# Optimization experiments

Measured on AMD Instinct MI355X. Metric: run time of the kernel, lower is better.

Reference implementation:

```python
import jax, jax.numpy as jnp
import numpy as np

N = 100_000   # nodes
E = 1_600_000 # edges (avg degree 16)
B = 512       # graphs in batch
F_IN = 64; H = 4; D = 64; HD = H * D; EXTRA = 16
NEG_SLOPE = 0.2  # DGL GATConv default


def _gat_conv(x, src, dst, W, al, ar, bias):
    """DGL GATConv: fc -> per-head attn logits -> edge leaky_relu -> segment softmax over dst -> scatter-sum."""
    h = (x @ W).reshape(N, H, D)                       # [N,H,D]
    el = jnp.sum(h * al, axis=-1)                      # [N,H]
    er = jnp.sum(h * ar, axis=-1)                      # [N,H]
    e = jax.nn.leaky_relu(el[src] + er[dst], NEG_SLOPE)  # [E,H]
    m = jax.ops.segment_max(e, dst, num_segments=N)    # [N,H]
    m = jnp.where(jnp.isfinite(m), m, 0.0)             # guard empty segments
    ex = jnp.exp(e - m[dst])                           # [E,H]
    den = jax.ops.segment_sum(ex, dst, num_segments=N) # [N,H]
    alpha = ex / jnp.maximum(den[dst], 1e-9)           # [E,H]
    msg = h[src] * alpha[:, :, None]                   # [E,H,D]
    out = jax.ops.segment_sum(msg, dst, num_segments=N) + bias.reshape(1, H, D)
    return out  # [N,H,D]


def setup_inputs() -> dict:
    key = jax.random.key(0)
    ks = jax.random.split(key, 26)
    nrm = lambda k, shape: jax.random.normal(k, shape, dtype=jnp.float32) * 0.5
    src = jax.random.randint(ks[0], (E,), 0, N)
    # ensure every node has >=1 incoming edge (DGL disallows zero in-degree by default)
    dst = jnp.concatenate([jnp.arange(N), jax.random.randint(ks[1], (E - N,), 0, N)])
    node_graph = jnp.sort(jax.random.randint(ks[2], (N,), 0, B))
    inp = dict(
        src=src, dst=dst, node_graph=node_graph,
        feats_node=jax.random.normal(ks[3], (N, F_IN), dtype=jnp.float32),
        feats_graph=jax.random.normal(ks[4], (B, EXTRA), dtype=jnp.float32),
        W1=nrm(ks[5], (F_IN, HD)), al1=nrm(ks[6], (H, D)), ar1=nrm(ks[7], (H, D)), bg1=jnp.zeros(HD),
        W2=nrm(ks[8], (HD, HD)),  al2=nrm(ks[9], (H, D)), ar2=nrm(ks[10], (H, D)), bg2=jnp.zeros(HD),
        W3=nrm(ks[11], (HD, HD)), al3=nrm(ks[12], (H, D)), ar3=nrm(ks[13], (H, D)), bg3=jnp.zeros(HD),
        sw=nrm(ks[14], (HD, 1)), sb=jnp.zeros(1),
        lw1=nrm(ks[15], (HD + EXTRA, 2 * D)), lb1=jnp.zeros(2 * D),
        lw2=nrm(ks[16], (2 * D, D)), lb2=jnp.zeros(D),
        lw3=nrm(ks[17], (D, 1)), lb3=jnp.zeros(1),
    )
    return inp


def reference(src, dst, node_graph, feats_node, feats_graph,
              W1, al1, ar1, bg1, W2, al2, ar2, bg2, W3, al3, ar3, bg3,
              sw, sb, lw1, lb1, lw2, lb2, lw3, lb3):
    selu = jax.nn.selu
    x = selu(_gat_conv(feats_node, src, dst, W1, al1, ar1, bg1)).reshape(N, HD)
    x = selu(_gat_conv(x, src, dst, W2, al2, ar2, bg2)).reshape(N, HD)
    x = selu(_gat_conv(x, src, dst, W3, al3, ar3, bg3)).reshape(N, HD)
    # WeightedAverage readout: sigmoid-scored weighted mean per graph
    w = jax.nn.sigmoid(x @ sw + sb)                               # [N,1]
    num = jax.ops.segment_sum(w * x, node_graph, num_segments=B)  # [B,HD]
    den = jax.ops.segment_sum(w, node_graph, num_segments=B)      # [B,1]
    emb = num / jnp.maximum(den, 1e-9)
    y = jnp.concatenate([emb, feats_graph], axis=1)
    y = selu(y @ lw1 + lb1)
    y = selu(y @ lw2 + lb2)
    return y @ lw3 + lb3  # [B,1]
```

## Files before the change

### kernel.cpp

```cpp
#include <hip/hip_runtime.h>

#define N_NODES 100000
#define N_EDGES 1600000
#define N_GRAPHS 512
#define F_IN 64
#define HD 256
#define EXTRA 16
#define SCAN_BLOCK 512

typedef float f32x4 __attribute__((ext_vector_type(4)));
typedef _Float16 f16x4 __attribute__((ext_vector_type(4)));
typedef _Float16 f16x8 __attribute__((ext_vector_type(8)));

__device__ __forceinline__ float selu_f(float x) {
    const float a = 1.6732632423543772f, sc = 1.0507009873554805f;
    return x > 0.f ? sc * x : sc * a * (__expf(x) - 1.f);
}

__global__ __launch_bounds__(256) void hist_k(const int* __restrict__ dst, int* __restrict__ hist) {
    int j = blockIdx.x * 256 + threadIdx.x;
    if (j < N_EDGES) atomicAdd(&hist[dst[j]], 1);
}

__global__ __launch_bounds__(SCAN_BLOCK) void scan1_k(const int* __restrict__ hist,
                                                      int* __restrict__ row_ptr,
                                                      int* __restrict__ bsums) {
    __shared__ int sm[SCAN_BLOCK];
    int t = threadIdx.x;
    int i = blockIdx.x * SCAN_BLOCK + t;
    int v = (i < N_NODES) ? hist[i] : 0;
    sm[t] = v;
    __syncthreads();
    for (int off = 1; off < SCAN_BLOCK; off <<= 1) {
        int add = (t >= off) ? sm[t - off] : 0;
        __syncthreads();
        sm[t] += add;
        __syncthreads();
    }
    if (i < N_NODES) row_ptr[i] = sm[t] - v;
    if (t == SCAN_BLOCK - 1) bsums[blockIdx.x] = sm[t];
}

__global__ __launch_bounds__(256) void scan2_k(int* __restrict__ bsums, int nb) {
    __shared__ int sm[256];
    int t = threadIdx.x;
    int v = (t < nb) ? bsums[t] : 0;
    sm[t] = v;
    __syncthreads();
    for (int off = 1; off < 256; off <<= 1) {
        int add = (t >= off) ? sm[t - off] : 0;
        __syncthreads();
        sm[t] += add;
        __syncthreads();
    }
    if (t < nb) bsums[t] = sm[t] - v;
}

__global__ __launch_bounds__(256) void scan3_k(int* __restrict__ row_ptr, const int* __restrict__ bsums,
                                               int* __restrict__ cursor) {
    int i = blockIdx.x * 256 + threadIdx.x;
    if (i < N_NODES) {
        int r = row_ptr[i] + bsums[i / SCAN_BLOCK];
        row_ptr[i] = r;
        cursor[i] = r;
    }
    if (i == 0) row_ptr[N_NODES] = N_EDGES;
}

__global__ __launch_bounds__(256) void scatter_k(const int* __restrict__ src,
                                                 const int* __restrict__ dst,
                                                 int* __restrict__ cursor,
                                                 int* __restrict__ csr_src) {
    int j = blockIdx.x * 256 + threadIdx.x;
    if (j < N_EDGES) {
        int r = atomicAdd(&cursor[dst[j]], 1);
        csr_src[r] = src[j];
    }
}

__global__ __launch_bounds__(256) void gbound_k(const int* __restrict__ node_graph, int* __restrict__ gstart) {
    int g = blockIdx.x * 256 + threadIdx.x;
    if (g > N_GRAPHS) return;
    int lo = 0, hi = N_NODES;
    while (lo < hi) {
        int mid = (lo + hi) >> 1;
        if (node_graph[mid] < g) lo = mid + 1; else hi = mid;
    }
    gstart[g] = lo;
}

__global__ __launch_bounds__(256) void tcast_split_k(const float* __restrict__ W,
                                                     _Float16* __restrict__ Wt_hi,
                                                     _Float16* __restrict__ Wt_lo, int K) {
    int idx = blockIdx.x * 256 + threadIdx.x;
    if (idx >= K * HD) return;
    int n = idx / K, k = idx - n * K;
    float w = W[(size_t)k * HD + n];
    _Float16 hi = (_Float16)w;
    _Float16 lo = (_Float16)(w - (float)hi);
    Wt_hi[idx] = hi;
    Wt_lo[idx] = lo;
}

__global__ __launch_bounds__(256) void split_cast_k(const float* __restrict__ in,
                                                    _Float16* __restrict__ hi,
                                                    _Float16* __restrict__ lo, int n4) {
    int i = blockIdx.x * 256 + threadIdx.x;
    if (i >= n4) return;
    float4 v = *(const float4*)(in + (size_t)i * 4);
    f16x4 h, l;
    h.x = (_Float16)v.x; l.x = (_Float16)(v.x - (float)h.x);
    h.y = (_Float16)v.y; l.y = (_Float16)(v.y - (float)h.y);
    h.z = (_Float16)v.z; l.z = (_Float16)(v.z - (float)h.z);
    h.w = (_Float16)v.w; l.w = (_Float16)(v.w - (float)h.w);
    *(f16x4*)(hi + (size_t)i * 4) = h;
    *(f16x4*)(lo + (size_t)i * 4) = l;
}

template <int K>
__global__ __launch_bounds__(256) void gemm_split_k(const _Float16* __restrict__ Ahi,
                                                    const _Float16* __restrict__ Alo,
                                                    const _Float16* __restrict__ Bt_hi,
                                                    const _Float16* __restrict__ Bt_lo,
                                                    const float* __restrict__ al,
                                                    const float* __restrict__ ar,
                                                    _Float16* __restrict__ Chi,
                                                    float* __restrict__ el,
                                                    float* __restrict__ er, int M) {
    const int BM = 128, BN = 128, LDP = 40;
    __shared__ _Float16 As_hi[BM][LDP];
    __shared__ _Float16 As_lo[BM][LDP];
    __shared__ _Float16 Bs_hi[BN][LDP];
    __shared__ _Float16 Bs_lo[BN][LDP];
    int tid = threadIdx.x;
    int wave = tid >> 6, lane = tid & 63;
    int q = lane >> 4, l16 = lane & 15;
    int row0 = blockIdx.y * BM, col0 = blockIdx.x * BN;
    f32x4 acc[2][8] = {};

    for (int k0 = 0; k0 < K; k0 += 32) {
#pragma unroll
        for (int c = 0; c < 2; c++) {
            int cc = tid + c * 256;
            int r = cc >> 2, o = (cc & 3) * 8;
            int gr = row0 + r;
            f16x8 vh = {}, vl = {};
            if (gr < M) {
                vh = *(const f16x8*)(Ahi + (size_t)gr * K + k0 + o);
                vl = *(const f16x8*)(Alo + (size_t)gr * K + k0 + o);
            }
            *(f16x8*)&As_hi[r][o] = vh;
            *(f16x8*)&As_lo[r][o] = vl;
        }
#pragma unroll
        for (int c = 0; c < 2; c++) {
            int cc = tid + c * 256;
            int n = cc >> 2, o = (cc & 3) * 8;
            *(f16x8*)&Bs_hi[n][o] = *(const f16x8*)(Bt_hi + (size_t)(col0 + n) * K + k0 + o);
            *(f16x8*)&Bs_lo[n][o] = *(const f16x8*)(Bt_lo + (size_t)(col0 + n) * K + k0 + o);
        }
        __syncthreads();

        f16x8 ah[2], alo2[2];
#pragma unroll
        for (int ms = 0; ms < 2; ms++) {
            int m = wave * 32 + ms * 16 + l16;
            ah[ms] = *(const f16x8*)&As_hi[m][q * 8];
            alo2[ms] = *(const f16x8*)&As_lo[m][q * 8];
        }
#pragma unroll
        for (int ns = 0; ns < 8; ns++) {
            int n = ns * 16 + l16;
            f16x8 bh = *(const f16x8*)&Bs_hi[n][q * 8];
            f16x8 bl = *(const f16x8*)&Bs_lo[n][q * 8];
#pragma unroll
            for (int ms = 0; ms < 2; ms++) {
                acc[ms][ns] = __builtin_amdgcn_mfma_f32_16x16x32_f16(ah[ms], bh, acc[ms][ns], 0, 0, 0);
                acc[ms][ns] = __builtin_amdgcn_mfma_f32_16x16x32_f16(ah[ms], bl, acc[ms][ns], 0, 0, 0);
                acc[ms][ns] = __builtin_amdgcn_mfma_f32_16x16x32_f16(alo2[ms], bh, acc[ms][ns], 0, 0, 0);
            }
        }
        __syncthreads();
    }

    const int h0 = col0 >> 6;
    float alv[8], arv[8];
#pragma unroll
    for (int ns = 0; ns < 8; ns++) {
        int hh = h0 + (ns >> 2);
        int d = (ns & 3) * 16 + l16;
        alv[ns] = al[hh * 64 + d];
        arv[ns] = ar[hh * 64 + d];
    }
#pragma unroll
    for (int ms = 0; ms < 2; ms++) {
#pragma unroll
        for (int i = 0; i < 4; i++) {
            int r = row0 + wave * 32 + ms * 16 + q * 4 + i;
            bool ok = r < M;
            float el0 = 0.f, er0 = 0.f, el1 = 0.f, er1 = 0.f;
#pragma unroll
            for (int ns = 0; ns < 8; ns++) {
                float v = acc[ms][ns][i];
                if (ok) Chi[(size_t)r * HD + col0 + ns * 16 + l16] = (_Float16)v;
                if (ns < 4) { el0 = fmaf(v, alv[ns], el0); er0 = fmaf(v, arv[ns], er0); }
                else        { el1 = fmaf(v, alv[ns], el1); er1 = fmaf(v, arv[ns], er1); }
            }
#pragma unroll
            for (int off = 1; off < 16; off <<= 1) {
                el0 += __shfl_xor(el0, off, 64);
                er0 += __shfl_xor(er0, off, 64);
                el1 += __shfl_xor(el1, off, 64);
                er1 += __shfl_xor(er1, off, 64);
            }
            if (l16 == 0 && ok) {
                el[(size_t)r * 4 + h0] = el0;
                el[(size_t)r * 4 + h0 + 1] = el1;
                er[(size_t)r * 4 + h0] = er0;
                er[(size_t)r * 4 + h0 + 1] = er1;
            }
        }
    }
}

template <int OUT>
__global__ __launch_bounds__(256) void gat_aggregate_k(const _Float16* __restrict__ hb,
                                                       const float* __restrict__ el,
                                                       const float* __restrict__ er,
                                                       const int* __restrict__ csr_src,
                                                       const int* __restrict__ row_ptr,
                                                       const float* __restrict__ bias,
                                                       _Float16* __restrict__ xhi,
                                                       _Float16* __restrict__ xlo,
                                                       float* __restrict__ xf32,
                                                       const float* __restrict__ sw,
                                                       const float* __restrict__ sb,
                                                       float* __restrict__ wsc) {
    __shared__ float wlds[4][64][4];
    __shared__ int snlds[4][64];
    int wv = threadIdx.x >> 6;
    int lane = threadIdx.x & 63;
    int v = blockIdx.x * 4 + wv;
    bool valid = v < N_NODES;
    int vc = valid ? v : 0;
    int rs = row_ptr[vc];
    int deg = valid ? row_ptr[vc + 1] - rs : 0;
    float4 erv = make_float4(0.f, 0.f, 0.f, 0.f);
    if (valid) erv = *(const float4*)(er + (size_t)vc * 4);

    int head = lane >> 4;
    float inv_den = 1.f;
    float m_h = 0.f, er_h = 0.f;
    f16x4 hv_pre[8];
    int nb0 = 0;

    if (deg <= 64) {
        float e0 = -1e30f, e1 = -1e30f, e2 = -1e30f, e3 = -1e30f;
        int my_sn = 0;
        if (lane < deg) {
            my_sn = csr_src[rs + lane];
            float4 elv = *(const float4*)(el + (size_t)my_sn * 4);
            float t0 = elv.x + erv.x, t1 = elv.y + erv.y, t2 = elv.z + erv.z, t3 = elv.w + erv.w;
            e0 = t0 > 0.f ? t0 : 0.2f * t0;
            e1 = t1 > 0.f ? t1 : 0.2f * t1;
            e2 = t2 > 0.f ? t2 : 0.2f * t2;
            e3 = t3 > 0.f ? t3 : 0.2f * t3;
        }
        nb0 = deg < 8 ? deg : 8;
#pragma unroll
        for (int u = 0; u < 8; u++) {
            int snb = __shfl(my_sn, u, 64);
            if (u < nb0) hv_pre[u] = *(const f16x4*)(hb + (size_t)snb * HD + lane * 4);
        }
        float m0 = e0, m1 = e1, m2 = e2, m3 = e3;
        for (int off = 1; off < deg; off <<= 1) {
            m0 = fmaxf(m0, __shfl_xor(m0, off, 64));
            m1 = fmaxf(m1, __shfl_xor(m1, off, 64));
            m2 = fmaxf(m2, __shfl_xor(m2, off, 64));
            m3 = fmaxf(m3, __shfl_xor(m3, off, 64));
        }
        float p0 = 0.f, p1 = 0.f, p2 = 0.f, p3 = 0.f;
        if (lane < deg) {
            p0 = __expf(e0 - m0); p1 = __expf(e1 - m1);
            p2 = __expf(e2 - m2); p3 = __expf(e3 - m3);
        }
        float s0 = p0, s1 = p1, s2 = p2, s3 = p3;
        for (int off = 1; off < deg; off <<= 1) {
            s0 += __shfl_xor(s0, off, 64);
            s1 += __shfl_xor(s1, off, 64);
            s2 += __shfl_xor(s2, off, 64);
            s3 += __shfl_xor(s3, off, 64);
        }
        float d0 = __shfl(s0, 0, 64), d1 = __shfl(s1, 0, 64);
        float d2 = __shfl(s2, 0, 64), d3 = __shfl(s3, 0, 64);
        float den = head == 0 ? d0 : head == 1 ? d1 : head == 2 ? d2 : d3;
        inv_den = 1.f / fmaxf(den, 1e-9f);
        if (lane < deg) {
            wlds[wv][lane][0] = p0;
            wlds[wv][lane][1] = p1;
            wlds[wv][lane][2] = p2;
            wlds[wv][lane][3] = p3;
            snlds[wv][lane] = my_sn;
        }
    } else {
        float m[4] = {-1e30f, -1e30f, -1e30f, -1e30f};
        float s[4] = {0.f, 0.f, 0.f, 0.f};
        for (int t = lane; t < deg; t += 64) {
            int sn = csr_src[rs + t];
            float4 elv = *(const float4*)(el + (size_t)sn * 4);
            float e[4];
            e[0] = elv.x + erv.x; e[1] = elv.y + erv.y; e[2] = elv.z + erv.z; e[3] = elv.w + erv.w;
#pragma unroll
            for (int hh = 0; hh < 4; hh++) {
                float ev = e[hh] > 0.f ? e[hh] : 0.2f * e[hh];
                float mn = fmaxf(m[hh], ev);
                s[hh] = s[hh] * __expf(m[hh] - mn) + __expf(ev - mn);
                m[hh] = mn;
            }
        }
#pragma unroll
        for (int off = 32; off >= 1; off >>= 1) {
#pragma unroll
            for (int hh = 0; hh < 4; hh++) {
                float mo = __shfl_xor(m[hh], off, 64);
                float so = __shfl_xor(s[hh], off, 64);
                float mn = fmaxf(m[hh], mo);
                s[hh] = s[hh] * __expf(m[hh] - mn) + so * __expf(mo - mn);
                m[hh] = mn;
            }
        }
        m_h = head == 0 ? m[0] : head == 1 ? m[1] : head == 2 ? m[2] : m[3];
        float den = head == 0 ? s[0] : head == 1 ? s[1] : head == 2 ? s[2] : s[3];
        er_h = head == 0 ? erv.x : head == 1 ? erv.y : head == 2 ? erv.z : erv.w;
        inv_den = 1.f / fmaxf(den, 1e-9f);
    }

    float a0 = 0.f, a1 = 0.f, a2 = 0.f, a3 = 0.f;
    if (deg <= 64) {
#pragma unroll
        for (int u = 0; u < 8; u++) {
            if (u < nb0) {
                float w = wlds[wv][u][head];
                a0 = fmaf(w, (float)hv_pre[u].x, a0);
                a1 = fmaf(w, (float)hv_pre[u].y, a1);
                a2 = fmaf(w, (float)hv_pre[u].z, a2);
                a3 = fmaf(w, (float)hv_pre[u].w, a3);
            }
        }
        int t = 8;
        for (; t + 8 <= deg; t += 8) {
            int sn[8];
            float w[8];
#pragma unroll
            for (int u = 0; u < 8; u++) {
                sn[u] = snlds[wv][t + u];
                w[u] = wlds[wv][t + u][head];
            }
            f16x4 hv[8];
#pragma unroll
            for (int u = 0; u < 8; u++)
                hv[u] = *(const f16x4*)(hb + (size_t)sn[u] * HD + lane * 4);
#pragma unroll
            for (int u = 0; u < 8; u++) {
                a0 = fmaf(w[u], (float)hv[u].x, a0);
                a1 = fmaf(w[u], (float)hv[u].y, a1);
                a2 = fmaf(w[u], (float)hv[u].z, a2);
                a3 = fmaf(w[u], (float)hv[u].w, a3);
            }
        }
        for (; t < deg; t++) {
            int sn = snlds[wv][t];
            float w = wlds[wv][t][head];
            f16x4 hv = *(const f16x4*)(hb + (size_t)sn * HD + lane * 4);
            a0 = fmaf(w, (float)hv.x, a0);
            a1 = fmaf(w, (float)hv.y, a1);
            a2 = fmaf(w, (float)hv.z, a2);
            a3 = fmaf(w, (float)hv.w, a3);
        }
    } else {
        for (int t = 0; t < deg; t++) {
            int sn = csr_src[rs + t];
            float e = el[(size_t)sn * 4 + head] + er_h;
            e = e > 0.f ? e : 0.2f * e;
            float w = __expf(e - m_h);
            f16x4 hv = *(const f16x4*)(hb + (size_t)sn * HD + lane * 4);
            a0 = fmaf(w, (float)hv.x, a0);
            a1 = fmaf(w, (float)hv.y, a1);
            a2 = fmaf(w, (float)hv.z, a2);
            a3 = fmaf(w, (float)hv.w, a3);
        }
    }
    float4 bv = *(const float4*)(bias + lane * 4);
    float4 o;
    o.x = selu_f(fmaf(a0, inv_den, bv.x));
    o.y = selu_f(fmaf(a1, inv_den, bv.y));
    o.z = selu_f(fmaf(a2, inv_den, bv.z));
    o.w = selu_f(fmaf(a3, inv_den, bv.w));

    if constexpr (OUT == 0) {
        f16x4 oh, ol;
        oh.x = (_Float16)o.x; ol.x = (_Float16)(o.x - (float)oh.x);
        oh.y = (_Float16)o.y; ol.y = (_Float16)(o.y - (float)oh.y);
        oh.z = (_Float16)o.z; ol.z = (_Float16)(o.z - (float)oh.z);
        oh.w = (_Float16)o.w; ol.w = (_Float16)(o.w - (float)oh.w);
        if (valid) {
            *(f16x4*)(xhi + (size_t)v * HD + lane * 4) = oh;
            *(f16x4*)(xlo + (size_t)v * HD + lane * 4) = ol;
        }
    } else {
        if (valid) *(float4*)(xf32 + (size_t)v * HD + lane * 4) = o;
        float4 sv = *(const float4*)(sw + lane * 4);
        float p = o.x * sv.x + o.y * sv.y + o.z * sv.z + o.w * sv.w;
#pragma unroll
        for (int off = 1; off < 64; off <<= 1) p += __shfl_xor(p, off, 64);
        if (lane == 0 && valid) wsc[v] = 1.f / (1.f + __expf(-(p + sb[0])));
    }
}

__global__ __launch_bounds__(256) void readout_k(const float* __restrict__ x,
                                                 const float* __restrict__ wsc,
                                                 const int* __restrict__ gstart,
                                                 const float* __restrict__ fg,
                                                 float* __restrict__ y0) {
    int g = blockIdx.x;
    int f = threadIdx.x;
    int s = gstart[g], e = gstart[g + 1];
    float num = 0.f, den = 0.f;
#pragma unroll 4
    for (int n = s; n < e; n++) {
        float wn = wsc[n];
        num = fmaf(wn, x[(size_t)n * HD + f], num);
        den += wn;
    }
    float emb = num / fmaxf(den, 1e-9f);
    y0[(size_t)g * 272 + f] = emb;
    if (f < EXTRA) y0[(size_t)g * 272 + 256 + f] = fg[g * EXTRA + f];
}

__global__ __launch_bounds__(128) void mlp_k(const float* __restrict__ y0g,
                                             const float* __restrict__ lw1, const float* __restrict__ lb1,
                                             const float* __restrict__ lw2, const float* __restrict__ lb2,
                                             const float* __restrict__ lw3, const float* __restrict__ lb3,
                                             float* __restrict__ out) {
    __shared__ float y0s[272];
    __shared__ float y1s[128];
    int g = blockIdx.x, t = threadIdx.x;
    for (int i = t; i < 272; i += 128) y0s[i] = y0g[(size_t)g * 272 + i];
    __syncthreads();
    float acc = lb1[t];
    for (int k = 0; k < 272; k++) acc = fmaf(y0s[k], lw1[k * 128 + t], acc);
    y1s[t] = selu_f(acc);
    __syncthreads();
    if (t < 64) {
        float a2 = lb2[t];
        for (int k = 0; k < 128; k++) a2 = fmaf(y1s[k], lw2[k * 64 + t], a2);
        float v2 = selu_f(a2);
        float p = v2 * lw3[t];
#pragma unroll
        for (int off = 1; off < 64; off <<= 1) p += __shfl_xor(p, off, 64);
        if (t == 0) out[g] = p + lb3[0];
    }
}

extern "C" void kernel_launch(void* const* d_in, const int* in_sizes, int n_in,
                              void* d_out, int out_size, void* d_ws, size_t ws_size,
                              hipStream_t stream) {
    const int* src = (const int*)d_in[0];
    const int* dst = (const int*)d_in[1];
    const int* node_graph = (const int*)d_in[2];
    const float* feats_node = (const float*)d_in[3];
    const float* feats_graph = (const float*)d_in[4];
    const float* W1 = (const float*)d_in[5];
    const float* al1 = (const float*)d_in[6];
    const float* ar1 = (const float*)d_in[7];
    const float* bg1 = (const float*)d_in[8];
    const float* W2 = (const float*)d_in[9];
    const float* al2 = (const float*)d_in[10];
    const float* ar2 = (const float*)d_in[11];
    const float* bg2 = (const float*)d_in[12];
    const float* W3 = (const float*)d_in[13];
    const float* al3 = (const float*)d_in[14];
    const float* ar3 = (const float*)d_in[15];
    const float* bg3 = (const float*)d_in[16];
    const float* sw = (const float*)d_in[17];
    const float* sb = (const float*)d_in[18];
    const float* lw1 = (const float*)d_in[19];
    const float* lb1 = (const float*)d_in[20];
    const float* lw2 = (const float*)d_in[21];
    const float* lb2 = (const float*)d_in[22];
    const float* lw3 = (const float*)d_in[23];
    const float* lb3 = (const float*)d_in[24];
    float* out = (float*)d_out;

    char* ws = (char*)d_ws;
    size_t off = 0;
    auto alloc = [&](size_t bytes) -> char* {
        char* p = ws + off;
        off += (bytes + 255) & ~(size_t)255;
        return p;
    };
    _Float16* xhi = (_Float16*)alloc((size_t)N_NODES * HD * 2);
    _Float16* xlo = (_Float16*)alloc((size_t)N_NODES * HD * 2);
    float* xf32 = (float*)xhi;
    _Float16* hhi = (_Float16*)alloc((size_t)N_NODES * HD * 2);
    _Float16* fhi = (_Float16*)alloc((size_t)N_NODES * F_IN * 2);
    _Float16* flo = (_Float16*)alloc((size_t)N_NODES * F_IN * 2);
    _Float16* W1hi = (_Float16*)alloc((size_t)F_IN * HD * 2);
    _Float16* W1lo = (_Float16*)alloc((size_t)F_IN * HD * 2);
    _Float16* W2hi = (_Float16*)alloc((size_t)HD * HD * 2);
    _Float16* W2lo = (_Float16*)alloc((size_t)HD * HD * 2);
    _Float16* W3hi = (_Float16*)alloc((size_t)HD * HD * 2);
    _Float16* W3lo = (_Float16*)alloc((size_t)HD * HD * 2);
    float* el = (float*)alloc((size_t)N_NODES * 4 * 4);
    float* er = (float*)alloc((size_t)N_NODES * 4 * 4);
    float* wsc = (float*)alloc((size_t)N_NODES * 4);
    float* y0 = (float*)alloc((size_t)N_GRAPHS * 272 * 4);
    int* hist = (int*)alloc((size_t)N_NODES * 4);
    int* row_ptr = (int*)alloc((size_t)(N_NODES + 1) * 4);
    int* cursor = (int*)alloc((size_t)N_NODES * 4);
    int* csr_src = (int*)alloc((size_t)N_EDGES * 4);
    int* gstart = (int*)alloc((size_t)(N_GRAPHS + 1) * 4);
    int* bsums = (int*)alloc(256 * 4);
    (void)ws_size; (void)in_sizes; (void)n_in; (void)out_size;

    hipMemsetAsync(hist, 0, (size_t)N_NODES * 4, stream);

    hist_k<<<(N_EDGES + 255) / 256, 256, 0, stream>>>(dst, hist);
    int nb = (N_NODES + SCAN_BLOCK - 1) / SCAN_BLOCK;
    scan1_k<<<nb, SCAN_BLOCK, 0, stream>>>(hist, row_ptr, bsums);
    scan2_k<<<1, 256, 0, stream>>>(bsums, nb);
    scan3_k<<<(N_NODES + 255) / 256, 256, 0, stream>>>(row_ptr, bsums, cursor);
    scatter_k<<<(N_EDGES + 255) / 256, 256, 0, stream>>>(src, dst, cursor, csr_src);
    gbound_k<<<3, 256, 0, stream>>>(node_graph, gstart);

    split_cast_k<<<(N_NODES * F_IN / 4 + 255) / 256, 256, 0, stream>>>(feats_node, fhi, flo, N_NODES * F_IN / 4);
    tcast_split_k<<<(F_IN * HD + 255) / 256, 256, 0, stream>>>(W1, W1hi, W1lo, F_IN);
    tcast_split_k<<<(HD * HD + 255) / 256, 256, 0, stream>>>(W2, W2hi, W2lo, HD);
    tcast_split_k<<<(HD * HD + 255) / 256, 256, 0, stream>>>(W3, W3hi, W3lo, HD);

    dim3 ggrid(HD / 128, (N_NODES + 127) / 128);
    int nwb = (N_NODES + 3) / 4;

    gemm_split_k<F_IN><<<ggrid, 256, 0, stream>>>(fhi, flo, W1hi, W1lo, al1, ar1, hhi, el, er, N_NODES);
    gat_aggregate_k<0><<<nwb, 256, 0, stream>>>(hhi, el, er, csr_src, row_ptr, bg1, xhi, xlo, nullptr, nullptr, nullptr, nullptr);
    gemm_split_k<HD><<<ggrid, 256, 0, stream>>>(xhi, xlo, W2hi, W2lo, al2, ar2, hhi, el, er, N_NODES);
    gat_aggregate_k<0><<<nwb, 256, 0, stream>>>(hhi, el, er, csr_src, row_ptr, bg2, xhi, xlo, nullptr, nullptr, nullptr, nullptr);
    gemm_split_k<HD><<<ggrid, 256, 0, stream>>>(xhi, xlo, W3hi, W3lo, al3, ar3, hhi, el, er, N_NODES);
    gat_aggregate_k<1><<<nwb, 256, 0, stream>>>(hhi, el, er, csr_src, row_ptr, bg3, nullptr, nullptr, xf32, sw, sb, wsc);

    readout_k<<<N_GRAPHS, 256, 0, stream>>>(xf32, wsc, gstart, feats_graph, y0);
    mlp_k<<<N_GRAPHS, 128, 0, stream>>>(y0, lw1, lb1, lw2, lb2, lw3, lb3, out);
}
```

Baseline: 952.8 us.

## Split wavefront into two half-waves gathering 16-byte neighbor rows per edge

The aggregation kernel now has each half of the 64-lane wavefront handle alternate edges, with each lane loading 8 fp16 features (16 bytes) per neighbor instead of 4. The two half-wave partial sums are combined with a cross-half shuffle, and the output stores are split between the halves. This doubles the edges in flight per wavefront and widens the per-lane gather loads, aimed at the latency-bound neighbor gather. In exchange it drops the explicit 8-edge prefetch that overlapped with the softmax reductions, and it doubles the accumulator registers.

```diff
diff --git a/kernel.cpp b/kernel.cpp
--- a/kernel.cpp
+++ b/kernel.cpp
@@ -240,6 +240,9 @@
     __shared__ int snlds[4][64];
     int wv = threadIdx.x >> 6;
     int lane = threadIdx.x & 63;
+    int p = lane >> 5;
+    int l = lane & 31;
+    int head_l = l >> 3;
     int v = blockIdx.x * 4 + wv;
     bool valid = v < N_NODES;
     int vc = valid ? v : 0;
@@ -248,13 +251,11 @@
     float4 erv = make_float4(0.f, 0.f, 0.f, 0.f);
     if (valid) erv = *(const float4*)(er + (size_t)vc * 4);
 
-    int head = lane >> 4;
     float inv_den = 1.f;
-    float m_h = 0.f, er_h = 0.f;
-    f16x4 hv_pre[8];
-    int nb0 = 0;
-
-    if (deg <= 64) {
+    bool fast = deg <= 64;
+    float acc[8] = {};
+
+    if (fast) {
         float e0 = -1e30f, e1 = -1e30f, e2 = -1e30f, e3 = -1e30f;
         int my_sn = 0;
         if (lane < deg) {
@@ -266,12 +267,6 @@
             e2 = t2 > 0.f ? t2 : 0.2f * t2;
             e3 = t3 > 0.f ? t3 : 0.2f * t3;
         }
-        nb0 = deg < 8 ? deg : 8;
-#pragma unroll
-        for (int u = 0; u < 8; u++) {
-            int snb = __shfl(my_sn, u, 64);
-            if (u < nb0) hv_pre[u] = *(const f16x4*)(hb + (size_t)snb * HD + lane * 4);
-        }
         float m0 = e0, m1 = e1, m2 = e2, m3 = e3;
         for (int off = 1; off < deg; off <<= 1) {
             m0 = fmaxf(m0, __shfl_xor(m0, off, 64));
@@ -293,7 +288,7 @@
         }
         float d0 = __shfl(s0, 0, 64), d1 = __shfl(s1, 0, 64);
         float d2 = __shfl(s2, 0, 64), d3 = __shfl(s3, 0, 64);
-        float den = head == 0 ? d0 : head == 1 ? d1 : head == 2 ? d2 : d3;
+        float den = head_l == 0 ? d0 : head_l == 1 ? d1 : head_l == 2 ? d2 : d3;
         inv_den = 1.f / fmaxf(den, 1e-9f);
         if (lane < deg) {
             wlds[wv][lane][0] = p0;
@@ -301,6 +296,19 @@
             wlds[wv][lane][2] = p2;
             wlds[wv][lane][3] = p3;
             snlds[wv][lane] = my_sn;
+        }
+
+#pragma unroll 8
+        for (int t = 0; t < deg; t += 2) {
+            int e = t + p;
+            bool act = e < deg;
+            int ei = act ? e : 0;
+            int sn = snlds[wv][ei];
+            float w = act ? wlds[wv][ei][head_l] : 0.f;
+            f16x8 hv = *(const f16x8*)(hb + (size_t)sn * HD + l * 8);
+#pragma unroll
+            for (int i = 0; i < 8; i++)
+                acc[i] = fmaf(w, (float)hv[i], acc[i]);
         }
     } else {
         float m[4] = {-1e30f, -1e30f, -1e30f, -1e30f};
@@ -329,91 +337,71 @@
                 m[hh] = mn;
             }
         }
-        m_h = head == 0 ? m[0] : head == 1 ? m[1] : head == 2 ? m[2] : m[3];
-        float den = head == 0 ? s[0] : head == 1 ? s[1] : head == 2 ? s[2] : s[3];
-        er_h = head == 0 ? erv.x : head == 1 ? erv.y : head == 2 ? erv.z : erv.w;
+        float m_h = head_l == 0 ? m[0] : head_l == 1 ? m[1] : head_l == 2 ? m[2] : m[3];
+        float den = head_l == 0 ? s[0] : head_l == 1 ? s[1] : head_l == 2 ? s[2] : s[3];
+        float er_h = head_l == 0 ? erv.x : head_l == 1 ? erv.y : head_l == 2 ? erv.z : erv.w;
         inv_den = 1.f / fmaxf(den, 1e-9f);
-    }
-
-    float a0 = 0.f, a1 = 0.f, a2 = 0.f, a3 = 0.f;
-    if (deg <= 64) {
-#pragma unroll
-        for (int u = 0; u < 8; u++) {
-            if (u < nb0) {
-                float w = wlds[wv][u][head];
-                a0 = fmaf(w, (float)hv_pre[u].x, a0);
-                a1 = fmaf(w, (float)hv_pre[u].y, a1);
-                a2 = fmaf(w, (float)hv_pre[u].z, a2);
-                a3 = fmaf(w, (float)hv_pre[u].w, a3);
-            }
-        }
-        int t = 8;
-        for (; t + 8 <= deg; t += 8) {
-            int sn[8];
-            float w[8];
-#pragma unroll
-            for (int u = 0; u < 8; u++) {
-                sn[u] = snlds[wv][t + u];
-                w[u] = wlds[wv][t + u][head];
-            }
-            f16x4 hv[8];
-#pragma unroll
-            for (int u = 0; u < 8; u++)
-                hv[u] = *(const f16x4*)(hb + (size_t)sn[u] * HD + lane * 4);
-#pragma unroll
-            for (int u = 0; u < 8; u++) {
-                a0 = fmaf(w[u], (float)hv[u].x, a0);
-                a1 = fmaf(w[u], (float)hv[u].y, a1);
-                a2 = fmaf(w[u], (float)hv[u].z, a2);
-                a3 = fmaf(w[u], (float)hv[u].w, a3);
-            }
-        }
-        for (; t < deg; t++) {
-            int sn = snlds[wv][t];
-            float w = wlds[wv][t][head];
-            f16x4 hv = *(const f16x4*)(hb + (size_t)sn * HD + lane * 4);
-            a0 = fmaf(w, (float)hv.x, a0);
-            a1 = fmaf(w, (float)hv.y, a1);
-            a2 = fmaf(w, (float)hv.z, a2);
-            a3 = fmaf(w, (float)hv.w, a3);
+        for (int t = 0; t < deg; t += 2) {
+            int e = t + p;
+            bool act = e < deg;
+            int sn = csr_src[rs + (act ? e : 0)];
+            float4 elv = *(const float4*)(el + (size_t)sn * 4);
+            float eh = (head_l == 0 ? elv.x : head_l == 1 ? elv.y : head_l == 2 ? elv.z : elv.w) + er_h;
+            eh = eh > 0.f ? eh : 0.2f * eh;
+            float w = act ? __expf(eh - m_h) : 0.f;
+            f16x8 hv = *(const f16x8*)(hb + (size_t)sn * HD + l * 8);
+#pragma unroll
+            for (int i = 0; i < 8; i++)
+                acc[i] = fmaf(w, (float)hv[i], acc[i]);
+        }
+    }
+
+#pragma unroll
+    for (int i = 0; i < 8; i++)
+        acc[i] += __shfl_xor(acc[i], 32, 64);
+
+    float4 b0 = *(const float4*)(bias + l * 8);
+    float4 b1 = *(const float4*)(bias + l * 8 + 4);
+    float o[8];
+    o[0] = selu_f(fmaf(acc[0], inv_den, b0.x));
+    o[1] = selu_f(fmaf(acc[1], inv_den, b0.y));
+    o[2] = selu_f(fmaf(acc[2], inv_den, b0.z));
+    o[3] = selu_f(fmaf(acc[3], inv_den, b0.w));
+    o[4] = selu_f(fmaf(acc[4], inv_den, b1.x));
+    o[5] = selu_f(fmaf(acc[5], inv_den, b1.y));
+    o[6] = selu_f(fmaf(acc[6], inv_den, b1.z));
+    o[7] = selu_f(fmaf(acc[7], inv_den, b1.w));
+
+    if constexpr (OUT == 0) {
+        if (valid) {
+            if (p == 0) {
+                f16x8 oh;
+#pragma unroll
+                for (int i = 0; i < 8; i++) oh[i] = (_Float16)o[i];
+                *(f16x8*)(xhi + (size_t)v * HD + l * 8) = oh;
+            } else {
+                f16x8 ol;
+#pragma unroll
+                for (int i = 0; i < 8; i++) {
+                    _Float16 h = (_Float16)o[i];
+                    ol[i] = (_Float16)(o[i] - (float)h);
+                }
+                *(f16x8*)(xlo + (size_t)v * HD + l * 8) = ol;
+            }
         }
     } else {
-        for (int t = 0; t < deg; t++) {
-            int sn = csr_src[rs + t];
-            float e = el[(size_t)sn * 4 + head] + er_h;
-            e = e > 0.f ? e : 0.2f * e;
-            float w = __expf(e - m_h);
-            f16x4 hv = *(const f16x4*)(hb + (size_t)sn * HD + lane * 4);
-            a0 = fmaf(w, (float)hv.x, a0);
-            a1 = fmaf(w, (float)hv.y, a1);
-            a2 = fmaf(w, (float)hv.z, a2);
-            a3 = fmaf(w, (float)hv.w, a3);
-        }
-    }
-    float4 bv = *(const float4*)(bias + lane * 4);
-    float4 o;
-    o.x = selu_f(fmaf(a0, inv_den, bv.x));
-    o.y = selu_f(fmaf(a1, inv_den, bv.y));
-    o.z = selu_f(fmaf(a2, inv_den, bv.z));
-    o.w = selu_f(fmaf(a3, inv_den, bv.w));
-
-    if constexpr (OUT == 0) {
-        f16x4 oh, ol;
-        oh.x = (_Float16)o.x; ol.x = (_Float16)(o.x - (float)oh.x);
-        oh.y = (_Float16)o.y; ol.y = (_Float16)(o.y - (float)oh.y);
-        oh.z = (_Float16)o.z; ol.z = (_Float16)(o.z - (float)oh.z);
-        oh.w = (_Float16)o.w; ol.w = (_Float16)(o.w - (float)oh.w);
         if (valid) {
-            *(f16x4*)(xhi + (size_t)v * HD + lane * 4) = oh;
-            *(f16x4*)(xlo + (size_t)v * HD + lane * 4) = ol;
-        }
-    } else {
-        if (valid) *(float4*)(xf32 + (size_t)v * HD + lane * 4) = o;
-        float4 sv = *(const float4*)(sw + lane * 4);
-        float p = o.x * sv.x + o.y * sv.y + o.z * sv.z + o.w * sv.w;
-#pragma unroll
-        for (int off = 1; off < 64; off <<= 1) p += __shfl_xor(p, off, 64);
-        if (lane == 0 && valid) wsc[v] = 1.f / (1.f + __expf(-(p + sb[0])));
+            if (p == 0)
+                *(float4*)(xf32 + (size_t)v * HD + l * 8) = make_float4(o[0], o[1], o[2], o[3]);
+            else
+                *(float4*)(xf32 + (size_t)v * HD + l * 8 + 4) = make_float4(o[4], o[5], o[6], o[7]);
+        }
+        float4 sv = *(const float4*)(sw + l * 8 + 4 * p);
+        float ps = p == 0 ? (o[0] * sv.x + o[1] * sv.y + o[2] * sv.z + o[3] * sv.w)
+                          : (o[4] * sv.x + o[5] * sv.y + o[6] * sv.z + o[7] * sv.w);
+#pragma unroll
+        for (int off = 1; off < 64; off <<= 1) ps += __shfl_xor(ps, off, 64);
+        if (lane == 0 && valid) wsc[v] = 1.f / (1.f + __expf(-(ps + sb[0])));
     }
 }
 
```

Measured after the change: 966.3 us. No clear change (+1.4%).

## Fuse weighted readout into final aggregation and register-prefetch GEMM tiles

Applied to the files above, without the earlier changes.

The final GAT aggregation now computes the sigmoid score and accumulates weighted node features and weights per graph with atomics, reducing in shared memory when all four nodes in a block share a graph. This removes the fp32 node-feature write, the gstart binary search and the separate readout kernel. Separately, the split-fp16 GEMM prefetches the next K tile into registers while MFMAs run on the current tile. Atomics make the float sums order-nondeterministic and add memsets, and the prefetch adds an extra barrier per K step.

```diff
diff --git a/kernel.cpp b/kernel.cpp
--- a/kernel.cpp
+++ b/kernel.cpp
@@ -76,17 +76,6 @@
         int r = atomicAdd(&cursor[dst[j]], 1);
         csr_src[r] = src[j];
     }
-}
-
-__global__ __launch_bounds__(256) void gbound_k(const int* __restrict__ node_graph, int* __restrict__ gstart) {
-    int g = blockIdx.x * 256 + threadIdx.x;
-    if (g > N_GRAPHS) return;
-    int lo = 0, hi = N_NODES;
-    while (lo < hi) {
-        int mid = (lo + hi) >> 1;
-        if (node_graph[mid] < g) lo = mid + 1; else hi = mid;
-    }
-    gstart[g] = lo;
 }
 
 __global__ __launch_bounds__(256) void tcast_split_k(const float* __restrict__ W,
@@ -138,28 +127,43 @@
     int row0 = blockIdx.y * BM, col0 = blockIdx.x * BN;
     f32x4 acc[2][8] = {};
 
-    for (int k0 = 0; k0 < K; k0 += 32) {
+    int sr = tid >> 2, so = (tid & 3) * 8;
+    f16x8 rAh[2], rAl[2], rBh[2], rBl[2];
+
+    auto load_tile = [&](int k0) {
 #pragma unroll
         for (int c = 0; c < 2; c++) {
-            int cc = tid + c * 256;
-            int r = cc >> 2, o = (cc & 3) * 8;
+            int r = sr + 64 * c;
             int gr = row0 + r;
             f16x8 vh = {}, vl = {};
             if (gr < M) {
-                vh = *(const f16x8*)(Ahi + (size_t)gr * K + k0 + o);
-                vl = *(const f16x8*)(Alo + (size_t)gr * K + k0 + o);
-            }
-            *(f16x8*)&As_hi[r][o] = vh;
-            *(f16x8*)&As_lo[r][o] = vl;
-        }
+                vh = *(const f16x8*)(Ahi + (size_t)gr * K + k0 + so);
+                vl = *(const f16x8*)(Alo + (size_t)gr * K + k0 + so);
+            }
+            rAh[c] = vh; rAl[c] = vl;
+            int gb = col0 + r;
+            rBh[c] = *(const f16x8*)(Bt_hi + (size_t)gb * K + k0 + so);
+            rBl[c] = *(const f16x8*)(Bt_lo + (size_t)gb * K + k0 + so);
+        }
+    };
+    auto store_tile = [&]() {
 #pragma unroll
         for (int c = 0; c < 2; c++) {
-            int cc = tid + c * 256;
-            int n = cc >> 2, o = (cc & 3) * 8;
-            *(f16x8*)&Bs_hi[n][o] = *(const f16x8*)(Bt_hi + (size_t)(col0 + n) * K + k0 + o);
-            *(f16x8*)&Bs_lo[n][o] = *(const f16x8*)(Bt_lo + (size_t)(col0 + n) * K + k0 + o);
-        }
-        __syncthreads();
+            int r = sr + 64 * c;
+            *(f16x8*)&As_hi[r][so] = rAh[c];
+            *(f16x8*)&As_lo[r][so] = rAl[c];
+            *(f16x8*)&Bs_hi[r][so] = rBh[c];
+            *(f16x8*)&Bs_lo[r][so] = rBl[c];
+        }
+    };
+
+    load_tile(0);
+    store_tile();
+    __syncthreads();
+
+    for (int k0 = 0; k0 < K; k0 += 32) {
+        bool more = (k0 + 32) < K;
+        if (more) load_tile(k0 + 32);
 
         f16x8 ah[2], alo2[2];
 #pragma unroll
@@ -180,7 +184,11 @@
                 acc[ms][ns] = __builtin_amdgcn_mfma_f32_16x16x32_f16(alo2[ms], bh, acc[ms][ns], 0, 0, 0);
             }
         }
-        __syncthreads();
+        if (more) {
+            __syncthreads();
+            store_tile();
+            __syncthreads();
+        }
     }
 
     const int h0 = col0 >> 6;
@@ -232,10 +240,11 @@
                                                        const float* __restrict__ bias,
                                                        _Float16* __restrict__ xhi,
                                                        _Float16* __restrict__ xlo,
-                                                       float* __restrict__ xf32,
                                                        const float* __restrict__ sw,
                                                        const float* __restrict__ sb,
-                                                       float* __restrict__ wsc) {
+                                                       const int* __restrict__ node_graph,
+                                                       float* __restrict__ num,
+                                                       float* __restrict__ den) {
     __shared__ float wlds[4][64][4];
     __shared__ int snlds[4][64];
     int wv = threadIdx.x >> 6;
@@ -293,8 +302,8 @@
         }
         float d0 = __shfl(s0, 0, 64), d1 = __shfl(s1, 0, 64);
         float d2 = __shfl(s2, 0, 64), d3 = __shfl(s3, 0, 64);
-        float den = head == 0 ? d0 : head == 1 ? d1 : head == 2 ? d2 : d3;
-        inv_den = 1.f / fmaxf(den, 1e-9f);
+        float dh = head == 0 ? d0 : head == 1 ? d1 : head == 2 ? d2 : d3;
+        inv_den = 1.f / fmaxf(dh, 1e-9f);
         if (lane < deg) {
             wlds[wv][lane][0] = p0;
             wlds[wv][lane][1] = p1;
@@ -330,9 +339,9 @@
             }
         }
         m_h = head == 0 ? m[0] : head == 1 ? m[1] : head == 2 ? m[2] : m[3];
-        float den = head == 0 ? s[0] : head == 1 ? s[1] : head == 2 ? s[2] : s[3];
+        float dh = head == 0 ? s[0] : head == 1 ? s[1] : head == 2 ? s[2] : s[3];
         er_h = head == 0 ? erv.x : head == 1 ? erv.y : head == 2 ? erv.z : erv.w;
-        inv_den = 1.f / fmaxf(den, 1e-9f);
+        inv_den = 1.f / fmaxf(dh, 1e-9f);
     }
 
     float a0 = 0.f, a1 = 0.f, a2 = 0.f, a3 = 0.f;
@@ -408,36 +417,40 @@
             *(f16x4*)(xlo + (size_t)v * HD + lane * 4) = ol;
         }
     } else {
-        if (valid) *(float4*)(xf32 + (size_t)v * HD + lane * 4) = o;
+        __shared__ float bnum[4][256];
+        __shared__ float bden[4];
+        __shared__ int bg[4];
         float4 sv = *(const float4*)(sw + lane * 4);
-        float p = o.x * sv.x + o.y * sv.y + o.z * sv.z + o.w * sv.w;
-#pragma unroll
-        for (int off = 1; off < 64; off <<= 1) p += __shfl_xor(p, off, 64);
-        if (lane == 0 && valid) wsc[v] = 1.f / (1.f + __expf(-(p + sb[0])));
-    }
-}
-
-__global__ __launch_bounds__(256) void readout_k(const float* __restrict__ x,
-                                                 const float* __restrict__ wsc,
-                                                 const int* __restrict__ gstart,
-                                                 const float* __restrict__ fg,
-                                                 float* __restrict__ y0) {
-    int g = blockIdx.x;
-    int f = threadIdx.x;
-    int s = gstart[g], e = gstart[g + 1];
-    float num = 0.f, den = 0.f;
-#pragma unroll 4
-    for (int n = s; n < e; n++) {
-        float wn = wsc[n];
-        num = fmaf(wn, x[(size_t)n * HD + f], num);
-        den += wn;
-    }
-    float emb = num / fmaxf(den, 1e-9f);
-    y0[(size_t)g * 272 + f] = emb;
-    if (f < EXTRA) y0[(size_t)g * 272 + 256 + f] = fg[g * EXTRA + f];
-}
-
-__global__ __launch_bounds__(128) void mlp_k(const float* __restrict__ y0g,
+        float ps = o.x * sv.x + o.y * sv.y + o.z * sv.z + o.w * sv.w;
+#pragma unroll
+        for (int off = 1; off < 64; off <<= 1) ps += __shfl_xor(ps, off, 64);
+        float wn = valid ? 1.f / (1.f + __expf(-(ps + sb[0]))) : 0.f;
+        int g = valid ? node_graph[vc] : -1;
+        bnum[wv][lane * 4 + 0] = wn * o.x;
+        bnum[wv][lane * 4 + 1] = wn * o.y;
+        bnum[wv][lane * 4 + 2] = wn * o.z;
+        bnum[wv][lane * 4 + 3] = wn * o.w;
+        if (lane == 0) { bden[wv] = wn; bg[wv] = g; }
+        __syncthreads();
+        bool uni = (bg[0] == bg[1]) && (bg[1] == bg[2]) && (bg[2] == bg[3]) && (bg[0] >= 0);
+        if (uni) {
+            int t = threadIdx.x;
+            float s = bnum[0][t] + bnum[1][t] + bnum[2][t] + bnum[3][t];
+            atomicAdd(&num[(size_t)bg[0] * 256 + t], s);
+            if (t == 0) atomicAdd(&den[bg[0]], bden[0] + bden[1] + bden[2] + bden[3]);
+        } else if (valid) {
+            atomicAdd(&num[(size_t)g * 256 + lane * 4 + 0], wn * o.x);
+            atomicAdd(&num[(size_t)g * 256 + lane * 4 + 1], wn * o.y);
+            atomicAdd(&num[(size_t)g * 256 + lane * 4 + 2], wn * o.z);
+            atomicAdd(&num[(size_t)g * 256 + lane * 4 + 3], wn * o.w);
+            if (lane == 0) atomicAdd(&den[g], wn);
+        }
+    }
+}
+
+__global__ __launch_bounds__(128) void mlp_k(const float* __restrict__ num,
+                                             const float* __restrict__ den,
+                                             const float* __restrict__ fg,
                                              const float* __restrict__ lw1, const float* __restrict__ lb1,
                                              const float* __restrict__ lw2, const float* __restrict__ lb2,
                                              const float* __restrict__ lw3, const float* __restrict__ lb3,
@@ -445,7 +458,9 @@
     __shared__ float y0s[272];
     __shared__ float y1s[128];
     int g = blockIdx.x, t = threadIdx.x;
-    for (int i = t; i < 272; i += 128) y0s[i] = y0g[(size_t)g * 272 + i];
+    float invden = 1.f / fmaxf(den[g], 1e-9f);
+    for (int i = t; i < 256; i += 128) y0s[i] = num[(size_t)g * 256 + i] * invden;
+    if (t < EXTRA) y0s[256 + t] = fg[g * EXTRA + t];
     __syncthreads();
     float acc = lb1[t];
     for (int k = 0; k < 272; k++) acc = fmaf(y0s[k], lw1[k * 128 + t], acc);
@@ -501,7 +516,6 @@
     };
     _Float16* xhi = (_Float16*)alloc((size_t)N_NODES * HD * 2);
     _Float16* xlo = (_Float16*)alloc((size_t)N_NODES * HD * 2);
-    float* xf32 = (float*)xhi;
     _Float16* hhi = (_Float16*)alloc((size_t)N_NODES * HD * 2);
     _Float16* fhi = (_Float16*)alloc((size_t)N_NODES * F_IN * 2);
     _Float16* flo = (_Float16*)alloc((size_t)N_NODES * F_IN * 2);
@@ -513,17 +527,18 @@
     _Float16* W3lo = (_Float16*)alloc((size_t)HD * HD * 2);
     float* el = (float*)alloc((size_t)N_NODES * 4 * 4);
     float* er = (float*)alloc((size_t)N_NODES * 4 * 4);
-    float* wsc = (float*)alloc((size_t)N_NODES * 4);
-    float* y0 = (float*)alloc((size_t)N_GRAPHS * 272 * 4);
+    float* num = (float*)alloc((size_t)N_GRAPHS * 256 * 4);
+    float* den = (float*)alloc((size_t)N_GRAPHS * 4);
     int* hist = (int*)alloc((size_t)N_NODES * 4);
     int* row_ptr = (int*)alloc((size_t)(N_NODES + 1) * 4);
     int* cursor = (int*)alloc((size_t)N_NODES * 4);
     int* csr_src = (int*)alloc((size_t)N_EDGES * 4);
-    int* gstart = (int*)alloc((size_t)(N_GRAPHS + 1) * 4);
     int* bsums = (int*)alloc(256 * 4);
     (void)ws_size; (void)in_sizes; (void)n_in; (void)out_size;
 
     hipMemsetAsync(hist, 0, (size_t)N_NODES * 4, stream);
+    hipMemsetAsync(num, 0, (size_t)N_GRAPHS * 256 * 4, stream);
+    hipMemsetAsync(den, 0, (size_t)N_GRAPHS * 4, stream);
 
     hist_k<<<(N_EDGES + 255) / 256, 256, 0, stream>>>(dst, hist);
     int nb = (N_NODES + SCAN_BLOCK - 1) / SCAN_BLOCK;
@@ -531,7 +546,6 @@
     scan2_k<<<1, 256, 0, stream>>>(bsums, nb);
     scan3_k<<<(N_NODES + 255) / 256, 256, 0, stream>>>(row_ptr, bsums, cursor);
     scatter_k<<<(N_EDGES + 255) / 256, 256, 0, stream>>>(src, dst, cursor, csr_src);
-    gbound_k<<<3, 256, 0, stream>>>(node_graph, gstart);
 
     split_cast_k<<<(N_NODES * F_IN / 4 + 255) / 256, 256, 0, stream>>>(feats_node, fhi, flo, N_NODES * F_IN / 4);
     tcast_split_k<<<(F_IN * HD + 255) / 256, 256, 0, stream>>>(W1, W1hi, W1lo, F_IN);
@@ -542,12 +556,11 @@
     int nwb = (N_NODES + 3) / 4;
 
     gemm_split_k<F_IN><<<ggrid, 256, 0, stream>>>(fhi, flo, W1hi, W1lo, al1, ar1, hhi, el, er, N_NODES);
-    gat_aggregate_k<0><<<nwb, 256, 0, stream>>>(hhi, el, er, csr_src, row_ptr, bg1, xhi, xlo, nullptr, nullptr, nullptr, nullptr);
+    gat_aggregate_k<0><<<nwb, 256, 0, stream>>>(hhi, el, er, csr_src, row_ptr, bg1, xhi, xlo, nullptr, nullptr, nullptr, nullptr, nullptr);
     gemm_split_k<HD><<<ggrid, 256, 0, stream>>>(xhi, xlo, W2hi, W2lo, al2, ar2, hhi, el, er, N_NODES);
-    gat_aggregate_k<0><<<nwb, 256, 0, stream>>>(hhi, el, er, csr_src, row_ptr, bg2, xhi, xlo, nullptr, nullptr, nullptr, nullptr);
+    gat_aggregate_k<0><<<nwb, 256, 0, stream>>>(hhi, el, er, csr_src, row_ptr, bg2, xhi, xlo, nullptr, nullptr, nullptr, nullptr, nullptr);
     gemm_split_k<HD><<<ggrid, 256, 0, stream>>>(xhi, xlo, W3hi, W3lo, al3, ar3, hhi, el, er, N_NODES);
-    gat_aggregate_k<1><<<nwb, 256, 0, stream>>>(hhi, el, er, csr_src, row_ptr, bg3, nullptr, nullptr, xf32, sw, sb, wsc);
-
-    readout_k<<<N_GRAPHS, 256, 0, stream>>>(xf32, wsc, gstart, feats_graph, y0);
-    mlp_k<<<N_GRAPHS, 128, 0, stream>>>(y0, lw1, lb1, lw2, lb2, lw3, lb3, out);
-}
+    gat_aggregate_k<1><<<nwb, 256, 0, stream>>>(hhi, el, er, csr_src, row_ptr, bg3, nullptr, nullptr, sw, sb, node_graph, num, den);
+
+    mlp_k<<<N_GRAPHS, 128, 0, stream>>>(num, den, feats_graph, lw1, lb1, lw2, lb2, lw3, lb3, out);
+}
```

Result: no change. 951.7 us (-0.1%).

## Use 2x2 wave tiling and register-prefetch next K tile in split GEMM

Applied to the files above, without the earlier changes.

The fp16 hi/lo split GEMM now gives each wave a 64x64 sub-tile (a 2x2 wave grid) instead of a 32x128 strip. This cuts LDS fragment reads per MFMA and makes each wave's el/er reduction cover a single head. The global loads for the next K slice are issued into registers before the current slice's MFMAs, then written to LDS between barriers, so load latency overlaps compute. The cost is more registers (16 accumulators plus prefetch buffers), which may lower occupancy.

```diff
diff --git a/kernel.cpp b/kernel.cpp
--- a/kernel.cpp
+++ b/kernel.cpp
@@ -134,90 +134,107 @@
     __shared__ _Float16 Bs_lo[BN][LDP];
     int tid = threadIdx.x;
     int wave = tid >> 6, lane = tid & 63;
+    int wr = wave >> 1, wc = wave & 1;
     int q = lane >> 4, l16 = lane & 15;
     int row0 = blockIdx.y * BM, col0 = blockIdx.x * BN;
-    f32x4 acc[2][8] = {};
-
-    for (int k0 = 0; k0 < K; k0 += 32) {
+    f32x4 acc[4][4] = {};
+
+    int sr = tid >> 2, so = (tid & 3) * 8;
+    f16x8 rAh[2], rAl[2], rBh[2], rBl[2];
+
+    auto load_tile = [&](int k0) {
 #pragma unroll
         for (int c = 0; c < 2; c++) {
-            int cc = tid + c * 256;
-            int r = cc >> 2, o = (cc & 3) * 8;
+            int r = sr + 64 * c;
             int gr = row0 + r;
             f16x8 vh = {}, vl = {};
             if (gr < M) {
-                vh = *(const f16x8*)(Ahi + (size_t)gr * K + k0 + o);
-                vl = *(const f16x8*)(Alo + (size_t)gr * K + k0 + o);
-            }
-            *(f16x8*)&As_hi[r][o] = vh;
-            *(f16x8*)&As_lo[r][o] = vl;
-        }
+                vh = *(const f16x8*)(Ahi + (size_t)gr * K + k0 + so);
+                vl = *(const f16x8*)(Alo + (size_t)gr * K + k0 + so);
+            }
+            rAh[c] = vh; rAl[c] = vl;
+            int gb = col0 + r;
+            rBh[c] = *(const f16x8*)(Bt_hi + (size_t)gb * K + k0 + so);
+            rBl[c] = *(const f16x8*)(Bt_lo + (size_t)gb * K + k0 + so);
+        }
+    };
+    auto store_tile = [&]() {
 #pragma unroll
         for (int c = 0; c < 2; c++) {
-            int cc = tid + c * 256;
-            int n = cc >> 2, o = (cc & 3) * 8;
-            *(f16x8*)&Bs_hi[n][o] = *(const f16x8*)(Bt_hi + (size_t)(col0 + n) * K + k0 + o);
-            *(f16x8*)&Bs_lo[n][o] = *(const f16x8*)(Bt_lo + (size_t)(col0 + n) * K + k0 + o);
-        }
-        __syncthreads();
-
-        f16x8 ah[2], alo2[2];
-#pragma unroll
-        for (int ms = 0; ms < 2; ms++) {
-            int m = wave * 32 + ms * 16 + l16;
-            ah[ms] = *(const f16x8*)&As_hi[m][q * 8];
-            alo2[ms] = *(const f16x8*)&As_lo[m][q * 8];
-        }
-#pragma unroll
-        for (int ns = 0; ns < 8; ns++) {
-            int n = ns * 16 + l16;
-            f16x8 bh = *(const f16x8*)&Bs_hi[n][q * 8];
-            f16x8 bl = *(const f16x8*)&Bs_lo[n][q * 8];
-#pragma unroll
-            for (int ms = 0; ms < 2; ms++) {
-                acc[ms][ns] = __builtin_amdgcn_mfma_f32_16x16x32_f16(ah[ms], bh, acc[ms][ns], 0, 0, 0);
-                acc[ms][ns] = __builtin_amdgcn_mfma_f32_16x16x32_f16(ah[ms], bl, acc[ms][ns], 0, 0, 0);
-                acc[ms][ns] = __builtin_amdgcn_mfma_f32_16x16x32_f16(alo2[ms], bh, acc[ms][ns], 0, 0, 0);
-            }
-        }
-        __syncthreads();
-    }
-
-    const int h0 = col0 >> 6;
-    float alv[8], arv[8];
-#pragma unroll
-    for (int ns = 0; ns < 8; ns++) {
-        int hh = h0 + (ns >> 2);
-        int d = (ns & 3) * 16 + l16;
-        alv[ns] = al[hh * 64 + d];
-        arv[ns] = ar[hh * 64 + d];
-    }
-#pragma unroll
-    for (int ms = 0; ms < 2; ms++) {
+            int r = sr + 64 * c;
+            *(f16x8*)&As_hi[r][so] = rAh[c];
+            *(f16x8*)&As_lo[r][so] = rAl[c];
+            *(f16x8*)&Bs_hi[r][so] = rBh[c];
+            *(f16x8*)&Bs_lo[r][so] = rBl[c];
+        }
+    };
+
+    load_tile(0);
+    store_tile();
+    __syncthreads();
+
+    for (int k0 = 0; k0 < K; k0 += 32) {
+        bool more = (k0 + 32) < K;
+        if (more) load_tile(k0 + 32);
+
+        f16x8 ah[4], alo2[4], bh[4], bl[4];
+#pragma unroll
+        for (int mf = 0; mf < 4; mf++) {
+            int m = wr * 64 + mf * 16 + l16;
+            ah[mf] = *(const f16x8*)&As_hi[m][q * 8];
+            alo2[mf] = *(const f16x8*)&As_lo[m][q * 8];
+        }
+#pragma unroll
+        for (int nf = 0; nf < 4; nf++) {
+            int n = wc * 64 + nf * 16 + l16;
+            bh[nf] = *(const f16x8*)&Bs_hi[n][q * 8];
+            bl[nf] = *(const f16x8*)&Bs_lo[n][q * 8];
+        }
+#pragma unroll
+        for (int mf = 0; mf < 4; mf++)
+#pragma unroll
+            for (int nf = 0; nf < 4; nf++) {
+                acc[mf][nf] = __builtin_amdgcn_mfma_f32_16x16x32_f16(ah[mf], bh[nf], acc[mf][nf], 0, 0, 0);
+                acc[mf][nf] = __builtin_amdgcn_mfma_f32_16x16x32_f16(ah[mf], bl[nf], acc[mf][nf], 0, 0, 0);
+                acc[mf][nf] = __builtin_amdgcn_mfma_f32_16x16x32_f16(alo2[mf], bh[nf], acc[mf][nf], 0, 0, 0);
+            }
+        if (more) {
+            __syncthreads();
+            store_tile();
+            __syncthreads();
+        }
+    }
+
+    const int hh = (col0 >> 6) + wc;
+    float alv[4], arv[4];
+#pragma unroll
+    for (int nf = 0; nf < 4; nf++) {
+        int d = nf * 16 + l16;
+        alv[nf] = al[hh * 64 + d];
+        arv[nf] = ar[hh * 64 + d];
+    }
+#pragma unroll
+    for (int mf = 0; mf < 4; mf++) {
 #pragma unroll
         for (int i = 0; i < 4; i++) {
-            int r = row0 + wave * 32 + ms * 16 + q * 4 + i;
+            int r = row0 + wr * 64 + mf * 16 + q * 4 + i;
             bool ok = r < M;
-            float el0 = 0.f, er0 = 0.f, el1 = 0.f, er1 = 0.f;
-#pragma unroll
-            for (int ns = 0; ns < 8; ns++) {
-                float v = acc[ms][ns][i];
-                if (ok) Chi[(size_t)r * HD + col0 + ns * 16 + l16] = (_Float16)v;
-                if (ns < 4) { el0 = fmaf(v, alv[ns], el0); er0 = fmaf(v, arv[ns], er0); }
-                else        { el1 = fmaf(v, alv[ns], el1); er1 = fmaf(v, arv[ns], er1); }
+            float e_l = 0.f, e_r = 0.f;
+#pragma unroll
+            for (int nf = 0; nf < 4; nf++) {
+                float v = acc[mf][nf][i];
+                if (ok) Chi[(size_t)r * HD + col0 + wc * 64 + nf * 16 + l16] = (_Float16)v;
+                e_l = fmaf(v, alv[nf], e_l);
+                e_r = fmaf(v, arv[nf], e_r);
             }
 #pragma unroll
             for (int off = 1; off < 16; off <<= 1) {
-                el0 += __shfl_xor(el0, off, 64);
-                er0 += __shfl_xor(er0, off, 64);
-                el1 += __shfl_xor(el1, off, 64);
-                er1 += __shfl_xor(er1, off, 64);
+                e_l += __shfl_xor(e_l, off, 64);
+                e_r += __shfl_xor(e_r, off, 64);
             }
             if (l16 == 0 && ok) {
-                el[(size_t)r * 4 + h0] = el0;
-                el[(size_t)r * 4 + h0 + 1] = el1;
-                er[(size_t)r * 4 + h0] = er0;
-                er[(size_t)r * 4 + h0 + 1] = er1;
+                el[(size_t)r * 4 + hh] = e_l;
+                er[(size_t)r * 4 + hh] = e_r;
             }
         }
     }
@@ -293,8 +310,8 @@
         }
         float d0 = __shfl(s0, 0, 64), d1 = __shfl(s1, 0, 64);
         float d2 = __shfl(s2, 0, 64), d3 = __shfl(s3, 0, 64);
-        float den = head == 0 ? d0 : head == 1 ? d1 : head == 2 ? d2 : d3;
-        inv_den = 1.f / fmaxf(den, 1e-9f);
+        float dh = head == 0 ? d0 : head == 1 ? d1 : head == 2 ? d2 : d3;
+        inv_den = 1.f / fmaxf(dh, 1e-9f);
         if (lane < deg) {
             wlds[wv][lane][0] = p0;
             wlds[wv][lane][1] = p1;
@@ -330,9 +347,9 @@
             }
         }
         m_h = head == 0 ? m[0] : head == 1 ? m[1] : head == 2 ? m[2] : m[3];
-        float den = head == 0 ? s[0] : head == 1 ? s[1] : head == 2 ? s[2] : s[3];
+        float dh = head == 0 ? s[0] : head == 1 ? s[1] : head == 2 ? s[2] : s[3];
         er_h = head == 0 ? erv.x : head == 1 ? erv.y : head == 2 ? erv.z : erv.w;
-        inv_den = 1.f / fmaxf(den, 1e-9f);
+        inv_den = 1.f / fmaxf(dh, 1e-9f);
     }
 
     float a0 = 0.f, a1 = 0.f, a2 = 0.f, a3 = 0.f;
```

Measured after the change: 965.2 us. No clear change (+1.3%).
